# Performance work log

Measured on AMD Instinct MI355X. Metric: run time of the kernel, lower is better.

Reference implementation:

```python
import jax, jax.numpy as jnp
import numpy as np

NS = 6   # stuff classes
NT = 4   # thing classes
B, N, H, W, ROI = 2, 32, 768, 768, 28
C = NS + NT
NEG = -100.0


def setup_inputs():
    key = jax.random.key(0)
    k1, k2, k3, k4, k5, k6, k7 = jax.random.split(key, 7)
    sem_logits = jax.random.normal(k1, (B, C, H, W), dtype=jnp.float32)
    roi_msk_logits = jax.random.normal(k2, (B, N, NT, ROI, ROI), dtype=jnp.float32)
    y0 = jax.random.uniform(k3, (B, N), minval=0.0, maxval=H - 240.0)
    x0 = jax.random.uniform(k4, (B, N), minval=0.0, maxval=W - 240.0)
    hb = jax.random.uniform(k5, (B, N), minval=40.0, maxval=200.0)
    wb = jax.random.uniform(k6, (B, N), minval=40.0, maxval=200.0)
    bbx = jnp.stack([y0, x0, y0 + hb, x0 + wb], axis=-1).astype(jnp.float32)
    cls = jax.random.randint(k7, (B, N), 0, NT, dtype=jnp.int32)
    return {"sem_logits": sem_logits, "roi_msk_logits": roi_msk_logits, "bbx": bbx, "cls": cls}


def _fuse_logits(sem_logits, roi_msk_logits, bbx, cls):
    """Float part of Pofusion_ONNX.forward -> po_logits [B, NS+N, H, W]."""
    Bb, Cc, Hh, Ww = sem_logits.shape
    Nn = bbx.shape[1]
    R = roi_msk_logits.shape[-1]
    yy = jnp.arange(Hh)
    xx = jnp.arange(Ww)
    # per-box mask logits of its predicted class: [B,N,R,R]
    msk = jnp.take_along_axis(roi_msk_logits, cls[:, :, None, None, None], axis=2)[:, :, 0]
    stuff = sem_logits[:, :NS]  # [B,NS,H,W]
    y0 = jnp.floor(bbx[..., 0]).astype(jnp.int32)
    x0 = jnp.floor(bbx[..., 1]).astype(jnp.int32)
    y1 = jnp.floor(bbx[..., 2]).astype(jnp.int32)
    x1 = jnp.floor(bbx[..., 3]).astype(jnp.int32)
    # ---- po_process_semantic_logits: instance canvas (uses round()+1 on max corner) ----
    y1r = (jnp.round(bbx[..., 2]) + 1.0).astype(jnp.int32)
    x1r = (jnp.round(bbx[..., 3]) + 1.0).astype(jnp.int32)
    in_y_s = (yy[None, None, :] >= y0[..., None]) & (yy[None, None, :] < y1r[..., None])  # [B,N,H]
    in_x_s = (xx[None, None, :] >= x0[..., None]) & (xx[None, None, :] < x1r[..., None])  # [B,N,W]
    thing_logit = jnp.take_along_axis(sem_logits, (cls + NS)[:, :, None, None], axis=1)   # [B,N,H,W]
    inst = jnp.where(in_y_s[:, :, :, None] & in_x_s[:, :, None, :], thing_logit, NEG)
    # ---- po_process_mask_logits: bilinear resize (align_corners=False) + paste ----
    h = jnp.maximum(y1 - y0 + 1, 1).astype(jnp.float32)
    w = jnp.maximum(x1 - x0 + 1, 1).astype(jnp.float32)
    ys = jnp.maximum(y0, 0); ye = jnp.minimum(y1 + 1, Hh)
    xs = jnp.maximum(x0, 0); xe = jnp.minimum(x1 + 1, Ww)
    in_y_m = (yy[None, None, :] >= ys[..., None]) & (yy[None, None, :] < ye[..., None])
    in_x_m = (xx[None, None, :] >= xs[..., None]) & (xx[None, None, :] < xe[..., None])
    # source coords, PyTorch half-pixel convention with lower clamp at 0
    sy = (yy[None, None, :].astype(jnp.float32) - y0[..., None] + 0.5) * (R / h[..., None]) - 0.5
    sx = (xx[None, None, :].astype(jnp.float32) - x0[..., None] + 0.5) * (R / w[..., None]) - 0.5
    sy = jnp.clip(sy, 0.0, R - 1.0)
    sx = jnp.clip(sx, 0.0, R - 1.0)
    iy0 = jnp.floor(sy).astype(jnp.int32); iy1 = jnp.minimum(iy0 + 1, R - 1); wy = sy - iy0
    ix0 = jnp.floor(sx).astype(jnp.int32); ix1 = jnp.minimum(ix0 + 1, R - 1); wx = sx - ix0
    # separable bilinear: rows first (cheap [B,N,H,R] intermediate), then columns
    m0 = jnp.take_along_axis(msk, iy0[:, :, :, None], axis=2)
    m1 = jnp.take_along_axis(msk, iy1[:, :, :, None], axis=2)
    m_y = m0 * (1.0 - wy[..., None]) + m1 * wy[..., None]          # [B,N,H,R]
    c0 = jnp.take_along_axis(m_y, ix0[:, :, None, :], axis=3)
    c1 = jnp.take_along_axis(m_y, ix1[:, :, None, :], axis=3)
    resized = c0 * (1.0 - wx[:, :, None, :]) + c1 * wx[:, :, None, :]  # [B,N,H,W]
    mask_canvas = jnp.where(in_y_m[:, :, :, None] & in_x_m[:, :, None, :], resized, NEG)
    combined = (jax.nn.sigmoid(inst) + jax.nn.sigmoid(mask_canvas)) * (inst + mask_canvas)
    return jnp.concatenate([stuff, combined], axis=1)  # [B, NS+N, H, W]


def _post(po_logits, sem_logits, cls):
    """po_assign_class_label + po_generate_seamless_output (min_stuff_area=0)."""
    b3 = jnp.arange(B)[:, None, None]
    b2 = jnp.arange(B)[:, None]
    po_pred = jnp.argmax(po_logits, axis=1)   # argmax(softmax) == argmax(logits)
    sem_pred = jnp.argmax(sem_logits, axis=1)
    thing = po_pred >= NS
    k = jnp.clip(po_pred - NS, 0, N - 1)      # instance (box) id per pixel
    # per-instance histogram of sem_pred over its region (regions are disjoint)
    hist = jnp.zeros((B, N, C), jnp.int32).at[b3, k, sem_pred].add(thing.astype(jnp.int32))
    total = hist.sum(-1)
    present = total > 0
    sem_max = jnp.argmax(hist, axis=-1).astype(jnp.int32)  # first max == torch unique order
    max_cnt = hist.max(-1)
    tmp = cls + NS
    br1 = sem_max == tmp
    br2 = (~br1) & (2 * max_cnt >= total) & (sem_max < NS) & present  # max/total >= 0.5
    sem_label = jnp.where(br2, sem_max, tmp)
    kept = present & ~br2
    idx = jnp.cumsum(present.astype(jnp.int32), axis=1) - 1  # rank among present ids
    inst_label = jnp.where(kept, idx, -1)
    po_sem = jnp.where(thing, sem_label[b3, k], po_pred.astype(jnp.int32))
    po_inst = jnp.where(thing, inst_label[b3, k], -1)
    # ---- seamless output ----
    sp = jnp.zeros((B, NS), jnp.int32).at[b3, jnp.clip(po_sem, 0, NS - 1)].add((po_sem < NS).astype(jnp.int32))
    stuff_present = sp > 0
    stuff_rank = jnp.cumsum(stuff_present.astype(jnp.int32), axis=1) - 1
    n_stuff = stuff_present.sum(1).astype(jnp.int32)  # [B]
    v = jnp.where(kept, idx, N)
    present_v = (jnp.zeros((B, N + 1), jnp.int32).at[b2, v].add(1) > 0)[:, :N]
    rank_v = jnp.cumsum(present_v.astype(jnp.int32), axis=1) - 1
    seam_inst = 1 + n_stuff[:, None, None] + rank_v[b3, jnp.clip(po_inst, 0, N - 1)]
    seam_stuff = stuff_rank[b3, jnp.clip(po_sem, 0, NS - 1)] + 1
    seam = jnp.where(po_inst >= 0, seam_inst, jnp.where(po_sem < NS, seam_stuff, 0))
    po_pred_seamless = seam.reshape(B * H, W).astype(jnp.int32)  # torch cat over batch
    # padded class list [255, sorted stuff classes..., kept instance classes...]
    L = 1 + NS + N
    po_cls = jnp.full((B, L + 1), -1, jnp.int32).at[:, 0].set(255)
    stuff_pos = jnp.where(stuff_present, 1 + stuff_rank, L)  # L = dump slot
    po_cls = po_cls.at[b2, stuff_pos].set(jnp.broadcast_to(jnp.arange(NS, dtype=jnp.int32), (B, NS)))
    rank_k = jnp.cumsum(kept.astype(jnp.int32), axis=1) - 1
    inst_pos = jnp.where(kept, 1 + n_stuff[:, None] + rank_k, L)
    po_cls = po_cls.at[b2, inst_pos].set(tmp)
    po_cls = po_cls[:, :L]
    valid_len = (1 + n_stuff + kept.sum(1)).astype(jnp.int32)
    po_iscrowd = jnp.where(jnp.arange(L)[None, :] < valid_len[:, None], 0, -1).astype(jnp.int32)
    return po_pred_seamless, po_cls, po_iscrowd, valid_len


def reference(sem_logits, roi_msk_logits, bbx, cls):
    po_logits = _fuse_logits(sem_logits, roi_msk_logits, bbx, cls)
    return _post(po_logits, sem_logits, cls)
```

## Files before the change

kernel.cpp:

```cpp
#include <hip/hip_runtime.h>
#include <math.h>

#define NSs 6
#define NTs 4
#define Bb  2
#define Nn  32
#define Hh  768
#define Ww  768
#define Rr  28
#define Cch 10
#define NCH 38
#define HW  (Hh*Ww)
#define NEGD (-100.0)
#define NKEY (Nn*Cch + NSs)

struct InstP {
  int y0, x0, y1r, x1r;
  int ys, ye, xs, xe;
  float sc_y, sc_x;
  int tc;
  int mskoff;
};

__device__ __forceinline__ double sigd(double x) { return 1.0 / (1.0 + exp(-x)); }

__device__ __forceinline__ int fuse_px(
    int y, int x, const float (&ch)[Cch], unsigned rel,
    const InstP* __restrict__ spar, const float* __restrict__ roi,
    double EPS, int* smp_out)
{
  int smp = 0; float smv = ch[0];
#pragma unroll
  for (int c = 1; c < Cch; c++) if (ch[c] > smv) { smv = ch[c]; smp = c; }
  *smp_out = smp;

  double m = (double)ch[0]; int pidx = 0;
#pragma unroll
  for (int c = 1; c < NSs; c++) { double v = (double)ch[c]; if (v > m) { m = v; pidx = c; } }

  int next_ch = NSs;
  while (rel) {
    int n = __ffs(rel) - 1; rel &= rel - 1;
    int chn_ = NSs + n;
    if (chn_ > next_ch && EPS > m) { m = EPS; pidx = next_ch; }
    next_ch = chn_ + 1;
    const InstP p = spar[n];
    bool in_i = (y >= p.y0) && (y < p.y1r) && (x >= p.x0) && (x < p.x1r);
    bool in_m = (y >= p.ys) && (y < p.ye)  && (x >= p.xs) && (x < p.xe);
    bool in_any = in_i || in_m;
    if (__any(in_any)) {
      if (in_any) {
        int tcl = p.tc;
        float tl = (tcl == 6) ? ch[6] : (tcl == 7) ? ch[7] : (tcl == 8) ? ch[8] : ch[9];
        double iv = in_i ? (double)tl : NEGD;
        double mv = NEGD;
        if (in_m) {
          double syv = ((double)(y - p.y0) + 0.5) * (double)p.sc_y - 0.5;
          double sxv = ((double)(x - p.x0) + 0.5) * (double)p.sc_x - 0.5;
          syv = fmin(fmax(syv, 0.0), 27.0);
          sxv = fmin(fmax(sxv, 0.0), 27.0);
          int iy0 = (int)syv, ix0 = (int)sxv;
          int iy1 = min(iy0 + 1, 27), ix1 = min(ix0 + 1, 27);
          double wy = syv - (double)iy0, wx = sxv - (double)ix0;
          const float* mp = roi + p.mskoff;
          double m00 = (double)mp[iy0*Rr + ix0];
          double m01 = (double)mp[iy0*Rr + ix1];
          double m10 = (double)mp[iy1*Rr + ix0];
          double m11 = (double)mp[iy1*Rr + ix1];
          double c0 = m00*(1.0 - wy) + m10*wy;
          double c1 = m01*(1.0 - wy) + m11*wy;
          mv = c0*(1.0 - wx) + c1*wx;
        }
        double s2 = iv + mv;
        if (fmax(2.0*s2, 0.0) > m) {
          double val = (sigd(iv) + sigd(mv)) * s2;
          if (val > m) { m = val; pidx = chn_; }
        }
      } else {
        if (EPS > m) { m = EPS; pidx = chn_; }
      }
    } else {
      if (EPS > m) { m = EPS; pidx = chn_; }
    }
  }
  if (next_ch < NCH && EPS > m) { m = EPS; pidx = next_ch; }
  return pidx;
}

__device__ __forceinline__ void setup_inst(
    int b, int n, const float* __restrict__ bbx, const int* __restrict__ cls,
    InstP* spar)
{
  const float* bbp = bbx + ((size_t)b*Nn + n)*4;
  float f0 = bbp[0], f1 = bbp[1], f2 = bbp[2], f3 = bbp[3];
  int y0 = (int)floorf(f0), x0 = (int)floorf(f1);
  int y1 = (int)floorf(f2), x1 = (int)floorf(f3);
  int y1r = (int)(rintf(f2) + 1.0f);
  int x1r = (int)(rintf(f3) + 1.0f);
  float hh = fmaxf((float)(y1 - y0 + 1), 1.0f);
  float wd = fmaxf((float)(x1 - x0 + 1), 1.0f);
  InstP p;
  p.y0 = y0; p.x0 = x0; p.y1r = y1r; p.x1r = x1r;
  p.ys = max(y0, 0); p.ye = min(y1 + 1, Hh);
  p.xs = max(x0, 0); p.xe = min(x1 + 1, Ww);
  p.sc_y = 28.0f / hh; p.sc_x = 28.0f / wd;
  int cl = cls[b*Nn + n];
  p.tc = NSs + cl;
  p.mskoff = (((b*Nn + n)*NTs) + cl)*Rr*Rr;
  spar[n] = p;
}

__global__ void k_zero(int* __restrict__ p, int n) {
  for (int i = threadIdx.x; i < n; i += 256) p[i] = 0;
}

__global__ __launch_bounds__(256) void k_fuse(
    const float* __restrict__ sem, const float* __restrict__ roi,
    const float* __restrict__ bbx, const int* __restrict__ cls,
    int* __restrict__ out_pred, int* __restrict__ g_hist, int* __restrict__ g_scount)
{
  __shared__ InstP spar[Nn];
  __shared__ int s_all[NKEY];
  __shared__ unsigned s_rel;
  __shared__ int s_xlo[Nn], s_xhi[Nn];

  const int bid  = blockIdx.x;
  const int y    = bid % Hh;
  const int b    = bid / Hh;
  const int tid  = threadIdx.x;
  const int lane = tid & 63;

  if (tid == 0) s_rel = 0u;
  for (int i = tid; i < NKEY; i += 256) s_all[i] = 0;
  if (tid < Nn) {
    setup_inst(b, tid, bbx, cls, spar);
    const InstP p = spar[tid];
    s_xlo[tid] = min(p.x0, p.xs);
    s_xhi[tid] = max(p.x1r, p.xe);
    bool rowi = (y >= p.y0) && (y < p.y1r);
    bool rowm = (y >= p.ys) && (y < p.ye);
    if (rowi || rowm) atomicOr(&s_rel, 1u << tid);
  }
  __syncthreads();

  const double EPS = (sigd(NEGD) + sigd(NEGD)) * (NEGD + NEGD);
  const float* base = sem + (size_t)b*Cch*HW + (size_t)y*Ww;

  const int  li   = lane & 31;
  const int  gxlo = s_xlo[li];
  const int  gxhi = s_xhi[li];
  const bool grow = (lane < 32) && ((s_rel >> li) & 1u);

  float cur[Cch], nxt[Cch];
#pragma unroll
  for (int c = 0; c < Cch; c++) cur[c] = base[(size_t)c*HW + tid];

  for (int ck = 0; ck < 3; ck++) {
    const int x = ck*256 + tid;
    if (ck < 2) {
#pragma unroll
      for (int c = 0; c < Cch; c++) nxt[c] = base[(size_t)c*HW + x + 256];
    }
    const int xa = x & ~63;
    unsigned relw = (unsigned)__ballot(grow && (gxlo < xa + 64) && (gxhi > xa));

    int smp;
    int pidx = fuse_px(y, x, cur, relw, spar, roi, EPS, &smp);
    out_pred[(size_t)b*HW + (size_t)y*Ww + x] = pidx;
    atomicAdd(&s_all[(pidx >= NSs) ? ((pidx - NSs)*Cch + smp) : (Nn*Cch + pidx)], 1);

    if (ck < 2) {
#pragma unroll
      for (int c = 0; c < Cch; c++) cur[c] = nxt[c];
    }
  }

  __syncthreads();
  for (int i = tid; i < NKEY; i += 256) {
    int v = s_all[i];
    if (v) {
      if (i < Nn*Cch) atomicAdd(&g_hist[b*Nn*Cch + i], v);
      else            atomicAdd(&g_scount[b*NSs + (i - Nn*Cch)], v);
    }
  }
}

__global__ __launch_bounds__(256) void k_seam2(
    int* __restrict__ pred, const int* __restrict__ g_hist,
    const int* __restrict__ g_scount, const int* __restrict__ cls,
    int* __restrict__ out_tail)
{
  __shared__ int sh[Bb*Nn*Cch];
  __shared__ int spc_f[Bb][NSs];
  __shared__ int pcf[Bb][40];
  __shared__ int slut[Bb*NCH];
  const int t = threadIdx.x;
  for (int i = t; i < Bb*Nn*Cch; i += 256) sh[i] = g_hist[i];
  if (t < Bb*NSs) spc_f[t/NSs][t%NSs] = g_scount[t];
  __syncthreads();

  const int  b    = t >> 6;
  const int  lane = t & 63;
  const int  bs   = b & 1;
  const bool bv   = b < Bb;
  const bool act  = bv && (lane < Nn);

  int total = 0, mi = 0, mx = -1, tmp = 0;
  bool br2 = false, kept = false;
  if (act) {
    const int* hb = sh + b*Nn*Cch + lane*Cch;
#pragma unroll
    for (int c = 0; c < Cch; c++) { int v = hb[c]; total += v; if (v > mx) { mx = v; mi = c; } }
    tmp = cls[b*Nn + lane] + NSs;
    bool present = total > 0;
    bool b1 = (mi == tmp);
    br2  = (!b1) && (2*mx >= total) && (mi < NSs) && present;
    kept = present && !br2;
    if (br2) atomicAdd(&spc_f[b][mi], total);
  }
  __syncthreads();

  unsigned mask6 = (unsigned)(__ballot(bv && lane < NSs && spc_f[bs][lane] > 0) & 0x3Full);
  int nstuff = __popc(mask6);
  unsigned kmask = (unsigned)(__ballot(act && kept) & 0xFFFFFFFFull);
  int nk = __popc(kmask);
  int vlen = 1 + nstuff + nk;

  if (bv && lane < NSs)
    slut[b*NCH + lane] = __popc(mask6 & ((1u << lane) - 1)) + 1;
  if (act) {
    int rk     = __popc(kmask & ((1u << lane) - 1));
    int srk_mi = __popc(mask6 & ((1u << mi) - 1));
    slut[b*NCH + NSs + lane] = kept ? (1 + nstuff + rk) : (br2 ? srk_mi + 1 : 0);
  }
  if (bv && lane < 39) pcf[b][lane] = -1;
  __syncthreads();
  if (bv && lane == 0) pcf[b][0] = 255;
  if (bv && lane < NSs && ((mask6 >> lane) & 1))
    pcf[b][1 + __popc(mask6 & ((1u << lane) - 1))] = lane;
  if (act && kept)
    pcf[b][1 + nstuff + __popc(kmask & ((1u << lane) - 1))] = tmp;
  __syncthreads();

  if (blockIdx.x == 0) {
    int* pc = out_tail;
    int* ic = out_tail + Bb*39;
    int* vl = out_tail + 2*Bb*39;
    if (bv && lane < 39) {
      pc[b*39 + lane] = pcf[b][lane];
      ic[b*39 + lane] = (lane < vlen) ? 0 : -1;
    }
    if (bv && lane == 0) vl[b] = vlen;
  }

  size_t i = ((size_t)blockIdx.x*256 + t) * 4;
  int bb = (int)(i / HW);
  int4 v = *reinterpret_cast<int4*>(pred + i);
  int bo = bb*NCH;
  v.x = slut[bo + v.x];
  v.y = slut[bo + v.y];
  v.z = slut[bo + v.z];
  v.w = slut[bo + v.w];
  *reinterpret_cast<int4*>(pred + i) = v;
}

extern "C" void kernel_launch(void* const* d_in, const int* in_sizes, int n_in,
                              void* d_out, int out_size, void* d_ws, size_t ws_size,
                              hipStream_t stream)
{
  const float* sem = (const float*)d_in[0];
  const float* roi = (const float*)d_in[1];
  const float* bbx = (const float*)d_in[2];
  const int*   cls = (const int*)d_in[3];
  int* out = (int*)d_out;

  int* g_hist   = (int*)d_ws;
  int* g_scount = g_hist + Bb*Nn*Cch;

  k_zero<<<1, 256, 0, stream>>>(g_hist, Bb*Nn*Cch + Bb*NSs);
  k_fuse<<<dim3(Bb*Hh), 256, 0, stream>>>(sem, roi, bbx, cls, out, g_hist, g_scount);
  k_seam2<<<dim3((Bb*HW)/(256*4)), 256, 0, stream>>>(out, g_hist, g_scount, cls,
                                                     out + (size_t)Bb*HW);
}
```

Measured before the change: 111.4 us.

## Add fp32 fast path for per-pixel argmax with double-precision fallback

Per-pixel fusion now runs first in fp32 with fast exp/divide intrinsics and tracks the gap between the winning score and the best exact and approximate runner-ups. Only when that margin falls below tolerance does it rerun the original double-precision path. The aim is to avoid costly fp64 exp and divide on most pixels. The cost is extra register pressure, some divergence, and a correctness risk if the tolerances are too small to cover fp32 error.

```diff
diff --git a/kernel.cpp b/kernel.cpp
--- a/kernel.cpp
+++ b/kernel.cpp
@@ -12,6 +12,7 @@
 #define NCH 38
 #define HW  (Hh*Ww)
 #define NEGD (-100.0)
+#define NEGF (-100.0f)
 #define NKEY (Nn*Cch + NSs)
 
 struct InstP {
@@ -23,6 +24,7 @@
 };
 
 __device__ __forceinline__ double sigd(double x) { return 1.0 / (1.0 + exp(-x)); }
+__device__ __forceinline__ float  sigf(float x)  { return __fdividef(1.0f, 1.0f + __expf(-x)); }
 
 __device__ __forceinline__ int fuse_px(
     int y, int x, const float (&ch)[Cch], unsigned rel,
@@ -87,6 +89,84 @@
   return pidx;
 }
 
+#define TOL_E 5e-4f
+#define TOL_A 1e-3f
+#define TOL_P 2e-3f
+
+__device__ __forceinline__ int fuse_px_f32(
+    int y, int x, const float (&ch)[Cch], unsigned rel,
+    const InstP* __restrict__ spar, const float* __restrict__ roi,
+    float EPSf, bool* certain)
+{
+  float m1 = ch[0]; int pidx = 0; bool wapprox = false;
+  float m2x = -1e30f, m2a = -1e30f;
+
+#define UPD_EXACT(v_, idx_) do { float _v = (v_); \
+    if (_v > m1) { if (wapprox) m2a = fmaxf(m2a, m1); else m2x = fmaxf(m2x, m1); \
+                   m1 = _v; pidx = (idx_); wapprox = false; } \
+    else m2x = fmaxf(m2x, _v); } while (0)
+#define UPD_APPROX(v_, idx_) do { float _v = (v_); \
+    if (_v > m1) { if (wapprox) m2a = fmaxf(m2a, m1); else m2x = fmaxf(m2x, m1); \
+                   m1 = _v; pidx = (idx_); wapprox = true; } \
+    else m2a = fmaxf(m2a, _v); } while (0)
+
+#pragma unroll
+  for (int c = 1; c < NSs; c++) UPD_EXACT(ch[c], c);
+
+  int next_ch = NSs;
+  while (rel) {
+    int n = __ffs(rel) - 1; rel &= rel - 1;
+    int chn_ = NSs + n;
+    if (chn_ > next_ch) UPD_EXACT(EPSf, next_ch);
+    next_ch = chn_ + 1;
+    const InstP p = spar[n];
+    bool in_i = (y >= p.y0) && (y < p.y1r) && (x >= p.x0) && (x < p.x1r);
+    bool in_m = (y >= p.ys) && (y < p.ye)  && (x >= p.xs) && (x < p.xe);
+    bool in_any = in_i || in_m;
+    if (__any(in_any)) {
+      if (in_any) {
+        int tcl = p.tc;
+        float tl = (tcl == 6) ? ch[6] : (tcl == 7) ? ch[7] : (tcl == 8) ? ch[8] : ch[9];
+        float iv = in_i ? tl : NEGF;
+        float mv = NEGF;
+        if (in_m) {
+          float syv = ((float)(y - p.y0) + 0.5f) * p.sc_y - 0.5f;
+          float sxv = ((float)(x - p.x0) + 0.5f) * p.sc_x - 0.5f;
+          syv = fminf(fmaxf(syv, 0.0f), 27.0f);
+          sxv = fminf(fmaxf(sxv, 0.0f), 27.0f);
+          int iy0 = (int)syv, ix0 = (int)sxv;
+          int iy1 = min(iy0 + 1, 27), ix1 = min(ix0 + 1, 27);
+          float wy = syv - (float)iy0, wx = sxv - (float)ix0;
+          const float* mp = roi + p.mskoff;
+          float m00 = mp[iy0*Rr + ix0];
+          float m01 = mp[iy0*Rr + ix1];
+          float m10 = mp[iy1*Rr + ix0];
+          float m11 = mp[iy1*Rr + ix1];
+          float c0 = m00*(1.0f - wy) + m10*wy;
+          float c1 = m01*(1.0f - wy) + m11*wy;
+          mv = c0*(1.0f - wx) + c1*wx;
+        }
+        float s2 = iv + mv;
+        if (fmaxf(2.0f*s2, 0.0f) > m1 - TOL_P) {
+          float val = (sigf(iv) + sigf(mv)) * s2;
+          UPD_APPROX(val, chn_);
+        }
+      } else {
+        UPD_EXACT(EPSf, chn_);
+      }
+    } else {
+      UPD_EXACT(EPSf, chn_);
+    }
+  }
+  if (next_ch < NCH) UPD_EXACT(EPSf, next_ch);
+
+  *certain = wapprox ? ((m1 - m2x > TOL_E) && (m1 - m2a > TOL_A))
+                     : (m1 - m2a > TOL_E);
+  return pidx;
+#undef UPD_EXACT
+#undef UPD_APPROX
+}
+
 __device__ __forceinline__ void setup_inst(
     int b, int n, const float* __restrict__ bbx, const int* __restrict__ cls,
     InstP* spar)
@@ -143,7 +223,8 @@
   }
   __syncthreads();
 
-  const double EPS = (sigd(NEGD) + sigd(NEGD)) * (NEGD + NEGD);
+  const double EPS  = (sigd(NEGD) + sigd(NEGD)) * (NEGD + NEGD);
+  const float  EPSf = (float)EPS;
   const float* base = sem + (size_t)b*Cch*HW + (size_t)y*Ww;
 
   const int  li   = lane & 31;
@@ -164,8 +245,16 @@
     const int xa = x & ~63;
     unsigned relw = (unsigned)__ballot(grow && (gxlo < xa + 64) && (gxhi > xa));
 
-    int smp;
-    int pidx = fuse_px(y, x, cur, relw, spar, roi, EPS, &smp);
+    bool certain;
+    int smp = 0;
+    int pidx = fuse_px_f32(y, x, cur, relw, spar, roi, EPSf, &certain);
+    if (!certain) {
+      pidx = fuse_px(y, x, cur, relw, spar, roi, EPS, &smp);
+    } else if (pidx >= NSs) {
+      float smv = cur[0];
+#pragma unroll
+      for (int c = 1; c < Cch; c++) if (cur[c] > smv) { smv = cur[c]; smp = c; }
+    }
     out_pred[(size_t)b*HW + (size_t)y*Ww + x] = pidx;
     atomicAdd(&s_all[(pidx >= NSs) ? ((pidx - NSs)*Cch + smp) : (Nn*Cch + pidx)], 1);
 
```

Measured after the change: 111.6 us. About the same (+0.2%).
